# Optimization experiments

Measured on AMD Instinct MI355X. Metric: run time of the kernel, lower is better.

## Reference

```python
import jax, jax.numpy as jnp
import numpy as np

# Assumed sub-module definitions (NODETracker repo, sources not provided):
#   MLP(in,out)   = Linear -> LayerNorm -> LeakyReLU(0.1)
#   MLPODEF(dim,hidden,n_layers=2) = Linear(dim->h) -> tanh -> [Linear(h->h) -> tanh]*(n_layers-1) -> Linear(h->dim)
#   ode_solver_factory(None) -> fixed-step RK4, here 4 steps over t in [0,1]

LEAKY = 0.1
N_ODE_STEPS = 4
LATENT_DIM = 512
OBS_DIM = 256
HID_DIM = 1024
STATE = 2 * LATENT_DIM  # 1024
TIME_LEN = 128
BATCH = 512


def mlp_block(x, W, b, g, beta):
    h = x @ W + b
    mu = h.mean(-1, keepdims=True)
    var = ((h - mu) ** 2).mean(-1, keepdims=True)
    h = (h - mu) * jax.lax.rsqrt(var + 1e-5) * g + beta
    return jnp.where(h >= 0, h, LEAKY * h)


def odef(z, p):
    W0, b0, W1, b1, W2, b2 = p
    h = jnp.tanh(z @ W0 + b0)
    h = jnp.tanh(h @ W1 + b1)
    return h @ W2 + b2


def rk4_solve(z, p):
    dt = 1.0 / N_ODE_STEPS
    def step(z, _):
        k1 = odef(z, p)
        k2 = odef(z + 0.5 * dt * k1, p)
        k3 = odef(z + 0.5 * dt * k2, p)
        k4 = odef(z + dt * k3, p)
        return z + (dt / 6.0) * (k1 + 2 * k2 + 2 * k3 + k4), None
    z, _ = jax.lax.scan(step, z, None, length=N_ODE_STEPS)
    return z


def gru_step(x, h, W_ih, W_hh, b_ih, b_hh):
    gi = x @ W_ih.T + b_ih
    gh = h @ W_hh.T + b_hh
    i_r, i_z, i_n = jnp.split(gi, 3, axis=-1)
    h_r, h_z, h_n = jnp.split(gh, 3, axis=-1)
    r = jax.nn.sigmoid(i_r + h_r)
    zg = jax.nn.sigmoid(i_z + h_z)
    n = jnp.tanh(i_n + r * h_n)
    return (1.0 - zg) * n + zg * h


def setup_inputs() -> dict:
    key = jax.random.key(0)
    ks = jax.random.split(key, 16)
    def lin(k, fi, fo):
        return jax.random.normal(k, (fi, fo), jnp.float32) / np.sqrt(fi)
    return {
        'xs': jax.random.normal(ks[0], (TIME_LEN, BATCH, OBS_DIM), jnp.float32),
        'obs_W': lin(ks[1], OBS_DIM, HID_DIM), 'obs_b': jnp.zeros((HID_DIM,), jnp.float32),
        'obs_g': jnp.ones((HID_DIM,), jnp.float32), 'obs_beta': jnp.zeros((HID_DIM,), jnp.float32),
        'lat_W': lin(ks[2], HID_DIM, STATE), 'lat_b': jnp.zeros((STATE,), jnp.float32),
        'lat_g': jnp.ones((STATE,), jnp.float32), 'lat_beta': jnp.zeros((STATE,), jnp.float32),
        'ode_W0': lin(ks[3], STATE, HID_DIM), 'ode_b0': jnp.zeros((HID_DIM,), jnp.float32),
        'ode_W1': lin(ks[4], HID_DIM, HID_DIM), 'ode_b1': jnp.zeros((HID_DIM,), jnp.float32),
        'ode_W2': lin(ks[5], HID_DIM, STATE), 'ode_b2': jnp.zeros((STATE,), jnp.float32),
        'gru_Wih': jax.random.normal(ks[6], (3 * STATE, STATE), jnp.float32) / np.sqrt(STATE),
        'gru_Whh': jax.random.normal(ks[7], (3 * STATE, STATE), jnp.float32) / np.sqrt(STATE),
        'gru_bih': jnp.zeros((3 * STATE,), jnp.float32),
        'gru_bhh': jnp.zeros((3 * STATE,), jnp.float32),
    }


def reference(xs, obs_W, obs_b, obs_g, obs_beta, lat_W, lat_b, lat_g, lat_beta,
              ode_W0, ode_b0, ode_W1, ode_b1, ode_W2, ode_b2,
              gru_Wih, gru_Whh, gru_bih, gru_bhh):
    hs = mlp_block(xs, obs_W, obs_b, obs_g, obs_beta)          # [T,B,hid]
    zs = mlp_block(hs, lat_W, lat_b, lat_g, lat_beta)          # [T,B,2*latent]
    ode_p = (ode_W0, ode_b0, ode_W1, ode_b1, ode_W2, ode_b2)
    batch = xs.shape[1]
    h0 = jnp.zeros((batch, STATE), xs.dtype)

    def step(h, z_t):
        z = rk4_solve(z_t, ode_p)                               # NODE solve from t=0 to 1
        h_new = gru_step(z, h, gru_Wih, gru_Whh, gru_bih, gru_bhh)
        return h_new, None

    z0, _ = jax.lax.scan(step, h0, zs)                          # [B,2*latent]
    return z0[:, :LATENT_DIM], z0[:, LATENT_DIM:]
```

## Files before the change

kernel.cpp:

```cpp
#include <hip/hip_runtime.h>
#include <hip/hip_bf16.h>
#include <hip/hip_cooperative_groups.h>

namespace cg = cooperative_groups;

typedef __bf16 bf16_t;
typedef __bf16 bf16x8 __attribute__((ext_vector_type(8)));
typedef float f32x4 __attribute__((ext_vector_type(4)));

#define TLEN 128
#define BATCHN 512
#define OBS 256
#define HID 1024
#define STATEDIM 1024
#define ROWS (TLEN * BATCHN)
#define RKDT 0.25f

enum { EPI_F32 = 0, EPI_GI, EPI_TANH, EPI_Z0, EPI_KG, EPI_K1, EPI_K2, EPI_K3, EPI_K4 };

__device__ __forceinline__ void gload_lds16(const bf16_t* g, bf16_t* l) {
  __builtin_amdgcn_global_load_lds(
      (const __attribute__((address_space(1))) void*)g,
      (__attribute__((address_space(3))) void*)l, 16, 0, 0);
}

__device__ __forceinline__ bf16_t f2bf(float x) { return (bf16_t)x; }

__device__ __forceinline__ float fast_tanh(float x) {
  const float e = __expf(2.f * x);
  return 1.f - 2.f / (e + 1.f);
}
__device__ __forceinline__ float fast_sigmoid(float x) {
  return 1.f / (1.f + __expf(-x));
}

#define MF(a_, b_, c_) __builtin_amdgcn_mfma_f32_16x16x32_bf16(a_, b_, c_, 0, 0, 0)

template<int EPI>
__global__ __launch_bounds__(256)
void gemm_bt(const bf16_t* __restrict__ A, const bf16_t* __restrict__ Wt,
             const float* __restrict__ bias, int M, int N, int K,
             float* __restrict__ outF, bf16_t* __restrict__ outB,
             float* __restrict__ Z, float* __restrict__ ZN,
             bf16_t* __restrict__ S2, const float* __restrict__ Z0,
             float kgc)
{
  __shared__ __align__(16) bf16_t As[2][128 * 32];
  __shared__ __align__(16) bf16_t Bs[2][128 * 32];
  const int tid = threadIdx.x;
  const int lane = tid & 63;
  const int wave = tid >> 6;
  const int nbn = N >> 7;

  int bid = blockIdx.x;
  {
    const int nwg = gridDim.x;
    const int q = nwg >> 3, r = nwg & 7;
    const int xcd = bid & 7, lid = bid >> 3;
    bid = (xcd < r ? xcd * (q + 1) : r * (q + 1) + (xcd - r) * q) + lid;
  }
  const int bm = bid / nbn;
  const int bn = bid % nbn;
  const int m0 = bm << 7, n0 = bn << 7;
  const int wr = wave >> 1, wc = wave & 1;
  const int srow = tid >> 2;
  const int scol = (tid & 3) << 3;

  f32x4 acc[4][4] = {};
  const int nk = K >> 5;
  int cur = 0;

  {
    const bf16_t* ga = A  + (size_t)(m0 + srow) * K + scol;
    const bf16_t* gb = Wt + (size_t)(n0 + srow) * K + scol;
    bf16_t* la = &As[0][tid * 8];
    bf16_t* lb = &Bs[0][tid * 8];
    gload_lds16(ga, la);
    gload_lds16(ga + (size_t)64 * K, la + 2048);
    gload_lds16(gb, lb);
    gload_lds16(gb + (size_t)64 * K, lb + 2048);
  }

  for (int ks = 0; ks < nk; ++ks) {
    __syncthreads();
    if (ks + 1 < nk) {
      const bf16_t* ga = A  + (size_t)(m0 + srow) * K + (ks + 1) * 32 + scol;
      const bf16_t* gb = Wt + (size_t)(n0 + srow) * K + (ks + 1) * 32 + scol;
      bf16_t* la = &As[cur ^ 1][tid * 8];
      bf16_t* lb = &Bs[cur ^ 1][tid * 8];
      gload_lds16(ga, la);
      gload_lds16(ga + (size_t)64 * K, la + 2048);
      gload_lds16(gb, lb);
      gload_lds16(gb + (size_t)64 * K, lb + 2048);
    }
    const int kb = (lane >> 4) << 3;
    const int rr = lane & 15;
    bf16x8 af[4], bfr[4];
#pragma unroll
    for (int i = 0; i < 4; ++i) {
      af[i]  = *(const bf16x8*)&As[cur][(wr * 64 + i * 16 + rr) * 32 + kb];
      bfr[i] = *(const bf16x8*)&Bs[cur][(wc * 64 + i * 16 + rr) * 32 + kb];
    }
#pragma unroll
    for (int i = 0; i < 4; ++i)
#pragma unroll
      for (int j = 0; j < 4; ++j)
        acc[i][j] = MF(af[i], bfr[j], acc[i][j]);
    cur ^= 1;
  }

  const int cb = n0 + wc * 64 + (lane & 15);
  const int rb = m0 + wr * 64 + ((lane >> 4) << 2);
#pragma unroll
  for (int j = 0; j < 4; ++j) {
    const int c = cb + j * 16;
    float bv = 0.f;
    if constexpr (EPI != EPI_F32 && EPI != EPI_KG) bv = bias[c];
#pragma unroll
    for (int i = 0; i < 4; ++i) {
      const int r0 = rb + i * 16;
#pragma unroll
      for (int r = 0; r < 4; ++r) {
        const size_t idx = (size_t)(r0 + r) * N + c;
        const float v = acc[i][j][r];
        if constexpr (EPI == EPI_F32) {
          outF[idx] = v;
        } else if constexpr (EPI == EPI_GI) {
          outF[idx] = v + bv;
        } else if constexpr (EPI == EPI_TANH) {
          outB[idx] = f2bf(fast_tanh(v + bv));
        } else if constexpr (EPI == EPI_Z0) {
          const float tz = v + bv;
          outF[idx] = tz;
          outB[idx] = f2bf(fast_tanh(tz));
        } else if constexpr (EPI == EPI_KG) {
          outB[idx] = f2bf(fast_tanh(Z0[idx] + kgc * v));
        } else if constexpr (EPI == EPI_K1) {
          const float k = v + bv;
          ZN[idx] = Z[idx] + (RKDT / 6.f) * k;
          outB[idx] = f2bf(k);
        } else if constexpr (EPI == EPI_K2 || EPI == EPI_K3) {
          const float k = v + bv;
          ZN[idx] += (RKDT / 3.f) * k;
          outB[idx] = f2bf(k);
        } else {
          const float k = v + bv;
          const float s = ZN[idx] + (RKDT / 6.f) * k;
          Z[idx] = s;
          const size_t si = (size_t)(r0 + r) * 2048 + c;
          const bf16_t hi = f2bf(s);
          S2[si] = hi;
          S2[si + 1024] = f2bf(s - (float)hi);
        }
      }
    }
  }
}

__global__ __launch_bounds__(512)
void gru_persistent(const float* __restrict__ gi,
                    const bf16_t* __restrict__ Whh,
                    const float* __restrict__ bhh,
                    float* __restrict__ Hf,
                    bf16_t* __restrict__ hb,
                    unsigned int* __restrict__ ctr,
                    float* __restrict__ outp,
                    int TS, int t0)
{
  __shared__ __align__(16) bf16_t Bs[48 * 1032];
  const int tid  = threadIdx.x;
  const int lane = tid & 63;
  const int w    = tid >> 6;
  const int rg   = blockIdx.x >> 6;
  const int jg   = blockIdx.x & 63;
  const int r0   = rg << 7;
  const int j0   = jg << 4;

  for (int it = tid; it < 48 * 128; it += 512) {
    const int rr = it >> 7;
    const int co = (it & 127) << 3;
    const int g = rr >> 4, c = rr & 15;
    *(bf16x8*)&Bs[rr * 1032 + co] =
        *(const bf16x8*)&Whh[(size_t)(g * 1024 + j0 + c) * 1024 + co];
  }

  const int myj = j0 + (lane & 15);
  const float bh_r = bhh[myj], bh_z = bhh[1024 + myj], bh_n = bhh[2048 + myj];
  const int rbase = r0 + w * 16 + ((lane >> 4) << 2);

  float h[4];
#pragma unroll
  for (int q = 0; q < 4; ++q) h[q] = Hf[(size_t)(rbase + q) * 1024 + myj];

  float gpre[12];
  auto load_gi = [&](int lt) {
    const float* gir = gi + (size_t)lt * 512 * 3072;
#pragma unroll
    for (int q = 0; q < 4; ++q) {
      const size_t rr = (size_t)(rbase + q);
      gpre[q * 3 + 0] = gir[rr * 3072 + myj];
      gpre[q * 3 + 1] = gir[rr * 3072 + 1024 + myj];
      gpre[q * 3 + 2] = gir[rr * 3072 + 2048 + myj];
    }
  };
  load_gi(0);

  __syncthreads();

  const int arow = r0 + w * 16 + (lane & 15);
  const int akoff = (lane >> 4) << 3;

  for (int s = 0; s < TS; ++s) {
    const int t = t0 + s;
    const bf16_t* ap = hb + (size_t)(t & 1) * 512 * 2048 +
                       (size_t)arow * 2048 + akoff;
    f32x4 a0 = {}, a1 = {}, a2 = {};
    const bf16_t* bp0 = &Bs[(0  + (lane & 15)) * 1032 + akoff];
    const bf16_t* bp1 = &Bs[(16 + (lane & 15)) * 1032 + akoff];
    const bf16_t* bp2 = &Bs[(32 + (lane & 15)) * 1032 + akoff];
#pragma unroll 8
    for (int kc = 0; kc < 64; ++kc) {
      const bf16x8 af = *(const bf16x8*)(ap + kc * 32);
      const int kl = (kc * 32) & 1023;
      a0 = MF(af, *(const bf16x8*)(bp0 + kl), a0);
      a1 = MF(af, *(const bf16x8*)(bp1 + kl), a1);
      a2 = MF(af, *(const bf16x8*)(bp2 + kl), a2);
    }
    bf16_t* hbw = hb + (size_t)((t + 1) & 1) * 512 * 2048;
#pragma unroll
    for (int q = 0; q < 4; ++q) {
      const size_t rr = (size_t)(rbase + q);
      const float rg_ = fast_sigmoid(gpre[q * 3 + 0] + a0[q] + bh_r);
      const float zg  = fast_sigmoid(gpre[q * 3 + 1] + a1[q] + bh_z);
      const float n   = fast_tanh(gpre[q * 3 + 2] + rg_ * (a2[q] + bh_n));
      h[q] = (1.f - zg) * n + zg * h[q];
      union { __bf16 b; unsigned short u; } uh, ul;
      uh.b = f2bf(h[q]);
      ul.b = f2bf(h[q] - (float)uh.b);
      const unsigned ph = (unsigned)__shfl_xor((int)uh.u, 1) & 0xFFFFu;
      const unsigned pl = (unsigned)__shfl_xor((int)ul.u, 1) & 0xFFFFu;
      if (!(lane & 1)) {
        const unsigned hiw = (unsigned)uh.u | (ph << 16);
        const unsigned low = (unsigned)ul.u | (pl << 16);
        __hip_atomic_store((unsigned*)(hbw + rr * 2048 + myj), hiw,
                           __ATOMIC_RELAXED, __HIP_MEMORY_SCOPE_AGENT);
        __hip_atomic_store((unsigned*)(hbw + rr * 2048 + 1024 + myj), low,
                           __ATOMIC_RELAXED, __HIP_MEMORY_SCOPE_AGENT);
      }
    }
    if (s + 1 < TS) load_gi(s + 1);

    __syncthreads();
    if (tid == 0) {
      __hip_atomic_fetch_add(ctr, 1u, __ATOMIC_RELAXED, __HIP_MEMORY_SCOPE_AGENT);
      const unsigned tgt = 256u * (unsigned)(s + 1);
      while (__hip_atomic_load(ctr, __ATOMIC_ACQUIRE, __HIP_MEMORY_SCOPE_AGENT) < tgt)
        __builtin_amdgcn_s_sleep(1);
    }
    __syncthreads();
  }

#pragma unroll
  for (int q = 0; q < 4; ++q) {
    const int r = rbase + q;
    Hf[(size_t)r * 1024 + myj] = h[q];
    if (myj < 512) outp[(size_t)r * 512 + myj] = h[q];
    else           outp[262144 + (size_t)r * 512 + (myj - 512)] = h[q];
  }
}

__global__ void gru_reset(unsigned int* ctr) {
  if (threadIdx.x == 0)
    __hip_atomic_store(ctr, 0u, __ATOMIC_RELAXED, __HIP_MEMORY_SCOPE_AGENT);
}

template<bool SPLIT>
__global__ __launch_bounds__(256)
void ln_leaky(const float* __restrict__ pre, const float* __restrict__ b,
              const float* __restrict__ g, const float* __restrict__ bet,
              bf16_t* __restrict__ outB, float* __restrict__ zf)
{
  const int row = blockIdx.x;
  const int tid = threadIdx.x;
  const float* p = pre + (size_t)row * 1024;
  float v[4];
  float s = 0.f, s2 = 0.f;
#pragma unroll
  for (int i = 0; i < 4; ++i) {
    const int c = tid + i * 256;
    v[i] = p[c] + b[c];
    s += v[i]; s2 += v[i] * v[i];
  }
#pragma unroll
  for (int o = 32; o; o >>= 1) { s += __shfl_down(s, o); s2 += __shfl_down(s2, o); }
  __shared__ float rs[4], rs2[4];
  if ((tid & 63) == 0) { rs[tid >> 6] = s; rs2[tid >> 6] = s2; }
  __syncthreads();
  s = rs[0] + rs[1] + rs[2] + rs[3];
  s2 = rs2[0] + rs2[1] + rs2[2] + rs2[3];
  const float mu = s * (1.f / 1024.f);
  const float var = s2 * (1.f / 1024.f) - mu * mu;
  const float rstd = rsqrtf(var + 1e-5f);
#pragma unroll
  for (int i = 0; i < 4; ++i) {
    const int c = tid + i * 256;
    float h = (v[i] - mu) * rstd * g[c] + bet[c];
    h = h >= 0.f ? h : 0.1f * h;
    if constexpr (SPLIT) {
      const bf16_t hi = f2bf(h);
      outB[(size_t)row * 2048 + c] = hi;
      outB[(size_t)row * 2048 + 1024 + c] = f2bf(h - (float)hi);
      zf[(size_t)row * 1024 + c] = h;
    } else {
      outB[(size_t)row * 1024 + c] = f2bf(h);
    }
  }
}

__global__ __launch_bounds__(256)
void transpose_bf16(const float* __restrict__ in, bf16_t* __restrict__ out, int R, int C)
{
  __shared__ float t[32][33];
  const int c0 = blockIdx.x * 32, r0 = blockIdx.y * 32;
  const int tx = threadIdx.x & 31, ty = threadIdx.x >> 5;
#pragma unroll
  for (int i = 0; i < 32; i += 8)
    t[ty + i][tx] = in[(size_t)(r0 + ty + i) * C + c0 + tx];
  __syncthreads();
#pragma unroll
  for (int i = 0; i < 32; i += 8)
    out[(size_t)(c0 + ty + i) * R + r0 + tx] = f2bf(t[tx][ty + i]);
}

__global__ __launch_bounds__(256)
void f2b_kernel(const float* __restrict__ in, bf16_t* __restrict__ out, int n)
{
  const int i = blockIdx.x * 256 + threadIdx.x;
  if (i < n) out[i] = f2bf(in[i]);
}

__global__ __launch_bounds__(256)
void dup2_kernel(const bf16_t* __restrict__ in, bf16_t* __restrict__ out, int N, int K)
{
  const int idx = blockIdx.x * 256 + threadIdx.x;
  if (idx >= N * 2 * K) return;
  const int n = idx / (2 * K);
  const int kk = idx - n * 2 * K;
  const int k = kk < K ? kk : kk - K;
  out[idx] = in[(size_t)n * K + k];
}

__global__ void sentinel_kernel(float* out, float code) {
  if (threadIdx.x == 0 && blockIdx.x == 0) out[0] = code;
}

extern "C" void kernel_launch(void* const* d_in, const int* in_sizes, int n_in,
                              void* d_out, int out_size, void* d_ws, size_t ws_size,
                              hipStream_t stream)
{
  const float* xs    = (const float*)d_in[0];
  const float* obs_W = (const float*)d_in[1];
  const float* obs_b = (const float*)d_in[2];
  const float* obs_g = (const float*)d_in[3];
  const float* obs_be= (const float*)d_in[4];
  const float* lat_W = (const float*)d_in[5];
  const float* lat_b = (const float*)d_in[6];
  const float* lat_g = (const float*)d_in[7];
  const float* lat_be= (const float*)d_in[8];
  const float* W0    = (const float*)d_in[9];
  const float* b0    = (const float*)d_in[10];
  const float* W1    = (const float*)d_in[11];
  const float* b1    = (const float*)d_in[12];
  const float* W2    = (const float*)d_in[13];
  const float* b2    = (const float*)d_in[14];
  const float* Wih   = (const float*)d_in[15];
  const float* Whh   = (const float*)d_in[16];
  const float* bih   = (const float*)d_in[17];
  const float* bhh   = (const float*)d_in[18];

  char* ws = (char*)d_ws;
  size_t off = 0;
  auto alloc = [&](size_t bytes) { char* p = ws + off; off += bytes; return p; };

  bf16_t* OBSWT = (bf16_t*)alloc((size_t)HID * OBS * 2);
  bf16_t* LATWT = (bf16_t*)alloc((size_t)STATEDIM * HID * 2);
  bf16_t* W0T   = (bf16_t*)alloc((size_t)HID * STATEDIM * 2);
  bf16_t* W0T2  = (bf16_t*)alloc((size_t)HID * 2048 * 2);
  bf16_t* W1T   = (bf16_t*)alloc((size_t)HID * HID * 2);
  bf16_t* W2T   = (bf16_t*)alloc((size_t)STATEDIM * HID * 2);
  bf16_t* WIH2  = (bf16_t*)alloc((size_t)3072 * 2048 * 2);
  bf16_t* WHHB  = (bf16_t*)alloc((size_t)3072 * 1024 * 2);
  float*  Hf    = (float*)alloc((size_t)512 * 1024 * 4);
  bf16_t* HB2   = (bf16_t*)alloc((size_t)2 * 512 * 2048 * 2);
  bf16_t* WIHB  = (bf16_t*)alloc((size_t)3072 * 1024 * 2);
  bf16_t* XSB   = (bf16_t*)alloc((size_t)ROWS * OBS * 2);
  unsigned int* CTR = (unsigned int*)alloc(128);
  const size_t staticEnd = off;

  int nc = -1;
  const int ncs[8] = {1, 2, 4, 8, 16, 32, 64, 128};
  for (int i = 0; i < 8; ++i) {
    const size_t R = (size_t)ROWS / ncs[i];
    if (staticEnd + R * 22528 <= ws_size) { nc = ncs[i]; break; }
  }
  if (nc < 0) {
    sentinel_kernel<<<1, 1, 0, stream>>>((float*)d_out,
                                         -(1000000.0f + (float)(ws_size >> 20)));
    return;
  }
  const int R = ROWS / nc;
  char* arena = ws + staticEnd;
  float*  A1f  = (float*)(arena);
  float*  A2f  = (float*)(arena + (size_t)R * 4096);
  float*  Z0f  = (float*)(arena + (size_t)R * 8192);
  bf16_t* H1b  = (bf16_t*)(arena + (size_t)R * 12288);
  bf16_t* H2b  = (bf16_t*)(arena + (size_t)R * 14336);
  bf16_t* KB   = (bf16_t*)(arena + (size_t)R * 16384);
  bf16_t* S2b  = (bf16_t*)(arena + (size_t)R * 18432);
  float*  GIf  = (float*)(arena);

  auto gemm = [&](int epi, const bf16_t* A, const bf16_t* Wt, const float* bias,
                  int M, int N, int K, float* oF, bf16_t* oB, float kgc = 0.f) {
    dim3 g((M / 128) * (N / 128)), b(256);
    switch (epi) {
      case EPI_F32:  gemm_bt<EPI_F32><<<g, b, 0, stream>>>(A, Wt, bias, M, N, K, oF, oB, A2f, A1f, S2b, Z0f, kgc); break;
      case EPI_GI:   gemm_bt<EPI_GI><<<g, b, 0, stream>>>(A, Wt, bias, M, N, K, oF, oB, A2f, A1f, S2b, Z0f, kgc); break;
      case EPI_TANH: gemm_bt<EPI_TANH><<<g, b, 0, stream>>>(A, Wt, bias, M, N, K, oF, oB, A2f, A1f, S2b, Z0f, kgc); break;
      case EPI_Z0:   gemm_bt<EPI_Z0><<<g, b, 0, stream>>>(A, Wt, bias, M, N, K, oF, oB, A2f, A1f, S2b, Z0f, kgc); break;
      case EPI_KG:   gemm_bt<EPI_KG><<<g, b, 0, stream>>>(A, Wt, bias, M, N, K, oF, oB, A2f, A1f, S2b, Z0f, kgc); break;
      case EPI_K1:   gemm_bt<EPI_K1><<<g, b, 0, stream>>>(A, Wt, bias, M, N, K, oF, oB, A2f, A1f, S2b, Z0f, kgc); break;
      case EPI_K2:   gemm_bt<EPI_K2><<<g, b, 0, stream>>>(A, Wt, bias, M, N, K, oF, oB, A2f, A1f, S2b, Z0f, kgc); break;
      case EPI_K3:   gemm_bt<EPI_K3><<<g, b, 0, stream>>>(A, Wt, bias, M, N, K, oF, oB, A2f, A1f, S2b, Z0f, kgc); break;
      case EPI_K4:   gemm_bt<EPI_K4><<<g, b, 0, stream>>>(A, Wt, bias, M, N, K, oF, oB, A2f, A1f, S2b, Z0f, kgc); break;
    }
  };

  transpose_bf16<<<dim3(HID / 32, OBS / 32), 256, 0, stream>>>(obs_W, OBSWT, OBS, HID);
  transpose_bf16<<<dim3(STATEDIM / 32, HID / 32), 256, 0, stream>>>(lat_W, LATWT, HID, STATEDIM);
  transpose_bf16<<<dim3(HID / 32, STATEDIM / 32), 256, 0, stream>>>(W0, W0T, STATEDIM, HID);
  dup2_kernel<<<(HID * 2048) / 256, 256, 0, stream>>>(W0T, W0T2, HID, 1024);
  transpose_bf16<<<dim3(HID / 32, HID / 32), 256, 0, stream>>>(W1, W1T, HID, HID);
  transpose_bf16<<<dim3(STATEDIM / 32, HID / 32), 256, 0, stream>>>(W2, W2T, HID, STATEDIM);
  f2b_kernel<<<(3072 * 1024) / 256, 256, 0, stream>>>(Wih, WIHB, 3072 * 1024);
  dup2_kernel<<<(3072 * 2048) / 256, 256, 0, stream>>>(WIHB, WIH2, 3072, 1024);
  f2b_kernel<<<(3072 * 1024) / 256, 256, 0, stream>>>(Whh, WHHB, 3072 * 1024);
  f2b_kernel<<<(ROWS * OBS) / 256, 256, 0, stream>>>(xs, XSB, ROWS * OBS);

  hipMemsetAsync(Hf, 0, (size_t)512 * 1024 * 4, stream);
  hipMemsetAsync(HB2, 0, (size_t)2 * 512 * 2048 * 2, stream);
  const int TS = R / BATCHN;

  for (int c = 0; c < nc; ++c) {
    gemm(EPI_F32, XSB + (size_t)c * R * OBS, OBSWT, nullptr, R, HID, OBS, A1f, nullptr);
    ln_leaky<false><<<R, 256, 0, stream>>>(A1f, obs_b, obs_g, obs_be, H1b, nullptr);
    gemm(EPI_F32, H1b, LATWT, nullptr, R, STATEDIM, HID, A1f, nullptr);
    ln_leaky<true><<<R, 256, 0, stream>>>(A1f, lat_b, lat_g, lat_be, S2b, A2f);

    for (int step = 0; step < 4; ++step) {
      gemm(EPI_Z0, S2b, W0T2, b0, R, HID, 2048, Z0f, H1b);
      gemm(EPI_TANH, H1b, W1T, b1, R, HID, HID, nullptr, H2b);
      gemm(EPI_K1, H2b, W2T, b2, R, STATEDIM, HID, nullptr, KB);
      for (int stg = 1; stg < 4; ++stg) {
        const float cg = (stg < 3) ? 0.5f * RKDT : RKDT;
        gemm(EPI_KG, KB, W0T, nullptr, R, HID, STATEDIM, nullptr, H1b, cg);
        gemm(EPI_TANH, H1b, W1T, b1, R, HID, HID, nullptr, H2b);
        gemm(EPI_K1 + stg, H2b, W2T, b2, R, STATEDIM, HID, nullptr, KB);
      }
    }

    gemm(EPI_GI, S2b, WIH2, bih, R, 3072, 2048, GIf, nullptr);

    gru_reset<<<1, 64, 0, stream>>>(CTR);
    {
      const float* giArg = GIf;
      const bf16_t* whhArg = WHHB;
      const float* bhhArg = bhh;
      float* hfArg = Hf;
      bf16_t* hbArg = HB2;
      unsigned int* ctrArg = CTR;
      float* outArg = (float*)d_out;
      int tsArg = TS;
      int t0Arg = c * TS;
      void* args[] = { (void*)&giArg, (void*)&whhArg, (void*)&bhhArg,
                       (void*)&hfArg, (void*)&hbArg, (void*)&ctrArg,
                       (void*)&outArg, (void*)&tsArg, (void*)&t0Arg };
      hipLaunchCooperativeKernel((const void*)gru_persistent,
                                 dim3(256), dim3(512), args, 0, stream);
    }
  }
}
```

Baseline: 18.91 ms.

## Update RK4 pre-activation incrementally and keep all k stages in bf16

For RK4 steps after the first, the first-layer pre-activation is updated incrementally: z0 += dz·W0, with dz stored in bf16. This replaces recomputing it from the hi/lo split state with K=2048, so that GEMM's K drops from 2048 to 1024. The k1..k3 stage outputs go to separate bf16 buffers and are combined in the K4 epilogue, instead of read-modify-writing an fp32 running sum after each stage. This cuts fp32 epilogue traffic, but quantising dz to bf16 and accumulating Z0 incrementally can drift from the precise two-part state.

```diff
diff --git a/kernel.cpp b/kernel.cpp
--- a/kernel.cpp
+++ b/kernel.cpp
@@ -16,7 +16,7 @@
 #define ROWS (TLEN * BATCHN)
 #define RKDT 0.25f
 
-enum { EPI_F32 = 0, EPI_GI, EPI_TANH, EPI_Z0, EPI_KG, EPI_K1, EPI_K2, EPI_K3, EPI_K4 };
+enum { EPI_F32 = 0, EPI_GI, EPI_TANH, EPI_Z0, EPI_Z0U, EPI_KW, EPI_KG, EPI_K4 };
 
 __device__ __forceinline__ void gload_lds16(const bf16_t* g, bf16_t* l) {
   __builtin_amdgcn_global_load_lds(
@@ -40,10 +40,12 @@
 __global__ __launch_bounds__(256)
 void gemm_bt(const bf16_t* __restrict__ A, const bf16_t* __restrict__ Wt,
              const float* __restrict__ bias, int M, int N, int K,
-             float* __restrict__ outF, bf16_t* __restrict__ outB,
-             float* __restrict__ Z, float* __restrict__ ZN,
-             bf16_t* __restrict__ S2, const float* __restrict__ Z0,
-             float kgc)
+             float* outF, bf16_t* __restrict__ outB,
+             float* Z, float* Z0,
+             bf16_t* S2,
+             const bf16_t* __restrict__ kb1, const bf16_t* __restrict__ kb2,
+             const bf16_t* __restrict__ kb3,
+             float kgc, int last)
 {
   __shared__ __align__(16) bf16_t As[2][128 * 32];
   __shared__ __align__(16) bf16_t Bs[2][128 * 32];
@@ -115,7 +117,7 @@
   for (int j = 0; j < 4; ++j) {
     const int c = cb + j * 16;
     float bv = 0.f;
-    if constexpr (EPI != EPI_F32 && EPI != EPI_KG) bv = bias[c];
+    if constexpr (EPI != EPI_F32 && EPI != EPI_KG && EPI != EPI_Z0U) bv = bias[c];
 #pragma unroll
     for (int i = 0; i < 4; ++i) {
       const int r0 = rb + i * 16;
@@ -133,24 +135,30 @@
           const float tz = v + bv;
           outF[idx] = tz;
           outB[idx] = f2bf(fast_tanh(tz));
+        } else if constexpr (EPI == EPI_Z0U) {
+          const float tz = Z0[idx] + v;
+          Z0[idx] = tz;
+          outB[idx] = f2bf(fast_tanh(tz));
+        } else if constexpr (EPI == EPI_KW) {
+          outB[idx] = f2bf(v + bv);
         } else if constexpr (EPI == EPI_KG) {
           outB[idx] = f2bf(fast_tanh(Z0[idx] + kgc * v));
-        } else if constexpr (EPI == EPI_K1) {
-          const float k = v + bv;
-          ZN[idx] = Z[idx] + (RKDT / 6.f) * k;
-          outB[idx] = f2bf(k);
-        } else if constexpr (EPI == EPI_K2 || EPI == EPI_K3) {
-          const float k = v + bv;
-          ZN[idx] += (RKDT / 3.f) * k;
-          outB[idx] = f2bf(k);
         } else {
-          const float k = v + bv;
-          const float s = ZN[idx] + (RKDT / 6.f) * k;
-          Z[idx] = s;
-          const size_t si = (size_t)(r0 + r) * 2048 + c;
-          const bf16_t hi = f2bf(s);
-          S2[si] = hi;
-          S2[si + 1024] = f2bf(s - (float)hi);
+          const float k4 = v + bv;
+          const float k1 = (float)kb1[idx];
+          const float k2 = (float)kb2[idx];
+          const float k3 = (float)kb3[idx];
+          const float dz = (RKDT / 6.f) * (k1 + 2.f * k2 + 2.f * k3 + k4);
+          const float zn = Z[idx] + dz;
+          Z[idx] = zn;
+          if (last) {
+            const size_t si = (size_t)(r0 + r) * 2048 + c;
+            const bf16_t hi = f2bf(zn);
+            S2[si] = hi;
+            S2[si + 1024] = f2bf(zn - (float)hi);
+          } else {
+            S2[idx] = f2bf(dz);
+          }
         }
       }
     }
@@ -411,27 +419,30 @@
   const int R = ROWS / nc;
   char* arena = ws + staticEnd;
   float*  A1f  = (float*)(arena);
-  float*  A2f  = (float*)(arena + (size_t)R * 4096);
+  bf16_t* KB1  = (bf16_t*)(arena);
+  bf16_t* KB2  = (bf16_t*)(arena + (size_t)R * 2048);
+  float*  Zf   = (float*)(arena + (size_t)R * 4096);
   float*  Z0f  = (float*)(arena + (size_t)R * 8192);
   bf16_t* H1b  = (bf16_t*)(arena + (size_t)R * 12288);
   bf16_t* H2b  = (bf16_t*)(arena + (size_t)R * 14336);
-  bf16_t* KB   = (bf16_t*)(arena + (size_t)R * 16384);
+  bf16_t* KB3  = (bf16_t*)(arena + (size_t)R * 16384);
   bf16_t* S2b  = (bf16_t*)(arena + (size_t)R * 18432);
+  bf16_t* DZb  = S2b;
   float*  GIf  = (float*)(arena);
 
   auto gemm = [&](int epi, const bf16_t* A, const bf16_t* Wt, const float* bias,
-                  int M, int N, int K, float* oF, bf16_t* oB, float kgc = 0.f) {
+                  int M, int N, int K, float* oF, bf16_t* oB,
+                  float kgc = 0.f, int last = 0) {
     dim3 g((M / 128) * (N / 128)), b(256);
     switch (epi) {
-      case EPI_F32:  gemm_bt<EPI_F32><<<g, b, 0, stream>>>(A, Wt, bias, M, N, K, oF, oB, A2f, A1f, S2b, Z0f, kgc); break;
-      case EPI_GI:   gemm_bt<EPI_GI><<<g, b, 0, stream>>>(A, Wt, bias, M, N, K, oF, oB, A2f, A1f, S2b, Z0f, kgc); break;
-      case EPI_TANH: gemm_bt<EPI_TANH><<<g, b, 0, stream>>>(A, Wt, bias, M, N, K, oF, oB, A2f, A1f, S2b, Z0f, kgc); break;
-      case EPI_Z0:   gemm_bt<EPI_Z0><<<g, b, 0, stream>>>(A, Wt, bias, M, N, K, oF, oB, A2f, A1f, S2b, Z0f, kgc); break;
-      case EPI_KG:   gemm_bt<EPI_KG><<<g, b, 0, stream>>>(A, Wt, bias, M, N, K, oF, oB, A2f, A1f, S2b, Z0f, kgc); break;
-      case EPI_K1:   gemm_bt<EPI_K1><<<g, b, 0, stream>>>(A, Wt, bias, M, N, K, oF, oB, A2f, A1f, S2b, Z0f, kgc); break;
-      case EPI_K2:   gemm_bt<EPI_K2><<<g, b, 0, stream>>>(A, Wt, bias, M, N, K, oF, oB, A2f, A1f, S2b, Z0f, kgc); break;
-      case EPI_K3:   gemm_bt<EPI_K3><<<g, b, 0, stream>>>(A, Wt, bias, M, N, K, oF, oB, A2f, A1f, S2b, Z0f, kgc); break;
-      case EPI_K4:   gemm_bt<EPI_K4><<<g, b, 0, stream>>>(A, Wt, bias, M, N, K, oF, oB, A2f, A1f, S2b, Z0f, kgc); break;
+      case EPI_F32:  gemm_bt<EPI_F32><<<g, b, 0, stream>>>(A, Wt, bias, M, N, K, oF, oB, Zf, Z0f, S2b, KB1, KB2, KB3, kgc, last); break;
+      case EPI_GI:   gemm_bt<EPI_GI><<<g, b, 0, stream>>>(A, Wt, bias, M, N, K, oF, oB, Zf, Z0f, S2b, KB1, KB2, KB3, kgc, last); break;
+      case EPI_TANH: gemm_bt<EPI_TANH><<<g, b, 0, stream>>>(A, Wt, bias, M, N, K, oF, oB, Zf, Z0f, S2b, KB1, KB2, KB3, kgc, last); break;
+      case EPI_Z0:   gemm_bt<EPI_Z0><<<g, b, 0, stream>>>(A, Wt, bias, M, N, K, oF, oB, Zf, Z0f, S2b, KB1, KB2, KB3, kgc, last); break;
+      case EPI_Z0U:  gemm_bt<EPI_Z0U><<<g, b, 0, stream>>>(A, Wt, bias, M, N, K, oF, oB, Zf, Z0f, S2b, KB1, KB2, KB3, kgc, last); break;
+      case EPI_KW:   gemm_bt<EPI_KW><<<g, b, 0, stream>>>(A, Wt, bias, M, N, K, oF, oB, Zf, Z0f, S2b, KB1, KB2, KB3, kgc, last); break;
+      case EPI_KG:   gemm_bt<EPI_KG><<<g, b, 0, stream>>>(A, Wt, bias, M, N, K, oF, oB, Zf, Z0f, S2b, KB1, KB2, KB3, kgc, last); break;
+      case EPI_K4:   gemm_bt<EPI_K4><<<g, b, 0, stream>>>(A, Wt, bias, M, N, K, oF, oB, Zf, Z0f, S2b, KB1, KB2, KB3, kgc, last); break;
     }
   };
 
@@ -454,18 +465,23 @@
     gemm(EPI_F32, XSB + (size_t)c * R * OBS, OBSWT, nullptr, R, HID, OBS, A1f, nullptr);
     ln_leaky<false><<<R, 256, 0, stream>>>(A1f, obs_b, obs_g, obs_be, H1b, nullptr);
     gemm(EPI_F32, H1b, LATWT, nullptr, R, STATEDIM, HID, A1f, nullptr);
-    ln_leaky<true><<<R, 256, 0, stream>>>(A1f, lat_b, lat_g, lat_be, S2b, A2f);
+    ln_leaky<true><<<R, 256, 0, stream>>>(A1f, lat_b, lat_g, lat_be, S2b, Zf);
 
     for (int step = 0; step < 4; ++step) {
-      gemm(EPI_Z0, S2b, W0T2, b0, R, HID, 2048, Z0f, H1b);
+      if (step == 0) gemm(EPI_Z0, S2b, W0T2, b0, R, HID, 2048, Z0f, H1b);
+      else           gemm(EPI_Z0U, DZb, W0T, nullptr, R, HID, 1024, nullptr, H1b);
       gemm(EPI_TANH, H1b, W1T, b1, R, HID, HID, nullptr, H2b);
-      gemm(EPI_K1, H2b, W2T, b2, R, STATEDIM, HID, nullptr, KB);
-      for (int stg = 1; stg < 4; ++stg) {
-        const float cg = (stg < 3) ? 0.5f * RKDT : RKDT;
-        gemm(EPI_KG, KB, W0T, nullptr, R, HID, STATEDIM, nullptr, H1b, cg);
-        gemm(EPI_TANH, H1b, W1T, b1, R, HID, HID, nullptr, H2b);
-        gemm(EPI_K1 + stg, H2b, W2T, b2, R, STATEDIM, HID, nullptr, KB);
-      }
+      gemm(EPI_KW, H2b, W2T, b2, R, STATEDIM, HID, nullptr, KB1);
+      gemm(EPI_KG, KB1, W0T, nullptr, R, HID, STATEDIM, nullptr, H1b, 0.5f * RKDT);
+      gemm(EPI_TANH, H1b, W1T, b1, R, HID, HID, nullptr, H2b);
+      gemm(EPI_KW, H2b, W2T, b2, R, STATEDIM, HID, nullptr, KB2);
+      gemm(EPI_KG, KB2, W0T, nullptr, R, HID, STATEDIM, nullptr, H1b, 0.5f * RKDT);
+      gemm(EPI_TANH, H1b, W1T, b1, R, HID, HID, nullptr, H2b);
+      gemm(EPI_KW, H2b, W2T, b2, R, STATEDIM, HID, nullptr, KB3);
+      gemm(EPI_KG, KB3, W0T, nullptr, R, HID, STATEDIM, nullptr, H1b, RKDT);
+      gemm(EPI_TANH, H1b, W1T, b1, R, HID, HID, nullptr, H2b);
+      gemm(EPI_K4, H2b, W2T, b2, R, STATEDIM, HID, nullptr, nullptr, 0.f,
+           (step == 3) ? 1 : 0);
     }
 
     gemm(EPI_GI, S2b, WIH2, bih, R, 3072, 2048, GIf, nullptr);
```

Result: no change. 18.83 ms (median of 4 runs) (-0.4%).
